# Kernel tuning notes

Hardware: AMD Instinct MI355X
Metric: run time of the kernel (lower is better)

## Reference

```python
import jax, jax.numpy as jnp
import numpy as np

N_NODES = 100000
N_EDGES = 1600000
D_IN = 128
D_HID = 128
N_CLS = 40


def setup_inputs() -> dict:
    key = jax.random.key(0)
    ks = jax.random.split(key, 8)
    x = jax.random.normal(ks[0], (N_NODES, D_IN), dtype=jnp.float32)
    edge_index = jax.random.randint(ks[1], (2, N_EDGES), 0, N_NODES, dtype=jnp.int64)
    s = 1.0 / np.sqrt(D_IN)
    W1_l = jax.random.normal(ks[2], (D_IN, D_HID), dtype=jnp.float32) * s
    W1_r = jax.random.normal(ks[3], (D_IN, D_HID), dtype=jnp.float32) * s
    b1 = jnp.zeros((D_HID,), dtype=jnp.float32)
    s2 = 1.0 / np.sqrt(D_HID)
    W2_l = jax.random.normal(ks[4], (D_HID, N_CLS), dtype=jnp.float32) * s2
    W2_r = jax.random.normal(ks[5], (D_HID, N_CLS), dtype=jnp.float32) * s2
    b2 = jnp.zeros((N_CLS,), dtype=jnp.float32)
    return {"x": x, "edge_index": edge_index, "W1_l": W1_l, "W1_r": W1_r,
            "b1": b1, "W2_l": W2_l, "W2_r": W2_r, "b2": b2}


def _sage_conv(x, src, dst, Wl, Wr, b):
    # mean-aggregate neighbor features (PyG SAGEConv, aggr='mean')
    n = x.shape[0]
    agg = jax.ops.segment_sum(x[src], dst, num_segments=n)           # [N, d]
    deg = jax.ops.segment_sum(jnp.ones_like(dst, dtype=x.dtype), dst, num_segments=n)
    mean = agg / jnp.maximum(deg, 1.0)[:, None]
    # lin_l(mean) + bias + lin_r(x_root)  (lin_r has no bias in PyG)
    return mean @ Wl + b + x @ Wr


def reference(x, edge_index, W1_l, W1_r, b1, W2_l, W2_r, b2):
    src, dst = edge_index[0], edge_index[1]
    h = jax.nn.relu(_sage_conv(x, src, dst, W1_l, W1_r, b1))
    # F.dropout(training=...) is identity in eval mode (deterministic reference)
    out = _sage_conv(h, src, dst, W2_l, W2_r, b2)
    return jax.nn.softmax(out, axis=1)
```

## Files before the change

### kernel.cpp

```cpp
#include <hip/hip_runtime.h>

#define DIM 128
#define NCLS 40
#define NBIN 256
#define BINSH 9
#define CHUNK 4096

typedef unsigned short ushort_t;
typedef __attribute__((ext_vector_type(8))) short bf16x8;
typedef __attribute__((ext_vector_type(4))) float f32x4;
typedef __attribute__((ext_vector_type(4))) unsigned uint4a;

__device__ __forceinline__ ushort_t f2b(float f) {
    union { float f; unsigned u; } v; v.f = f;
    unsigned r = v.u + 0x7FFFu + ((v.u >> 16) & 1u);
    return (ushort_t)(r >> 16);
}

__device__ __forceinline__ float b2f(ushort_t b) {
    union { unsigned u; float f; } v; v.u = ((unsigned)b) << 16;
    return v.f;
}

__device__ __forceinline__ void acc_fp8x4(float4& a, int w) {
    a.x += __builtin_amdgcn_cvt_f32_fp8(w, 0);
    a.y += __builtin_amdgcn_cvt_f32_fp8(w, 1);
    a.z += __builtin_amdgcn_cvt_f32_fp8(w, 2);
    a.w += __builtin_amdgcn_cvt_f32_fp8(w, 3);
}

__device__ __forceinline__ void acc_pair(float& a, float& b, unsigned u) {
    union { unsigned x; float f; } lo, hi;
    lo.x = u << 16;
    hi.x = u & 0xFFFF0000u;
    a += lo.f;
    b += hi.f;
}

__global__ __launch_bounds__(256) void prep_kernel(
    const float* __restrict__ x, ushort_t* __restrict__ xbf, unsigned* __restrict__ xq,
    const float* __restrict__ W1r, const float* __restrict__ W1l, ushort_t* __restrict__ Wp,
    const float* __restrict__ W2l, ushort_t* __restrict__ Wp2,
    int* __restrict__ binCnt, int n4, int cb)
{
    const int b = blockIdx.x;
    if (b < cb) {
        int i = b * 256 + threadIdx.x;
        if (i >= n4) return;
        f32x4 v = __builtin_nontemporal_load(((const f32x4*)x) + i);
        ushort4 o;
        o.x = f2b(v.x); o.y = f2b(v.y); o.z = f2b(v.z); o.w = f2b(v.w);
        ((ushort4*)xbf)[i] = o;
        int p = __builtin_amdgcn_cvt_pk_fp8_f32(v.x, v.y, 0, false);
        p = __builtin_amdgcn_cvt_pk_fp8_f32(v.z, v.w, p, true);
        xq[i] = (unsigned)p;
    } else if (b < cb + 128) {
        int o = (b - cb) * 256 + threadIdx.x;
        int j    = o & 7;
        int lane = (o >> 3) & 63;
        int t    = (o >> 9) & 7;
        int kc   = o >> 12;
        int k = kc * 32 + (lane >> 4) * 8 + j;
        int nn = t * 16 + (lane & 15);
        float v = (k < DIM) ? W1r[k * DIM + nn] : W1l[(k - DIM) * DIM + nn];
        Wp[o] = f2b(v);
    } else if (b < cb + 152) {
        int o = (b - cb - 128) * 256 + threadIdx.x;
        int j    = o & 7;
        int lane = (o >> 3) & 63;
        int rem  = o >> 9;
        int t    = rem % 3;
        int kc   = rem / 3;
        int k  = kc * 32 + (lane >> 4) * 8 + j;
        int nn = t * 16 + (lane & 15);
        Wp2[o] = (nn < NCLS) ? f2b(W2l[k * NCLS + nn]) : (ushort_t)0;
    } else {
        binCnt[threadIdx.x] = 0;
    }
}


__global__ __launch_bounds__(256) void bincount_kernel(const int* __restrict__ dst,
                                                       int* __restrict__ binCnt, int E) {
    __shared__ int hist[NBIN];
    hist[threadIdx.x] = 0;
    __syncthreads();
    const int tid = blockIdx.x * 256 + threadIdx.x;
    const int stride = gridDim.x * 256;
    for (int e = tid; e < E; e += stride)
        atomicAdd(&hist[__builtin_nontemporal_load(dst + e) >> BINSH], 1);
    __syncthreads();
    if (hist[threadIdx.x]) atomicAdd(&binCnt[threadIdx.x], hist[threadIdx.x]);
}

__global__ __launch_bounds__(NBIN) void binscan_kernel(const int* __restrict__ binCnt,
                                                       int* __restrict__ binBase,
                                                       int* __restrict__ binCtr,
                                                       int* __restrict__ row_ptr, int n) {
    __shared__ int sc[NBIN];
    const int t = threadIdx.x;
    sc[t] = binCnt[t];
    __syncthreads();
    for (int off = 1; off < NBIN; off <<= 1) {
        int v = (t >= off) ? sc[t - off] : 0;
        __syncthreads();
        sc[t] += v;
        __syncthreads();
    }
    int excl = (t == 0) ? 0 : sc[t - 1];
    binBase[t] = excl;
    binCtr[t]  = excl;
    if (t == NBIN - 1) { binBase[NBIN] = sc[t]; row_ptr[n] = sc[t]; }
}

__global__ __launch_bounds__(256) void binscatter_kernel(
    const int* __restrict__ src, const int* __restrict__ dst,
    int* __restrict__ binCtr, int2* __restrict__ pairs, int E)
{
    __shared__ int ss[CHUNK];
    __shared__ int sd[CHUNK];
    __shared__ int hist[NBIN];
    __shared__ int base[NBIN];
    __shared__ int cnt[NBIN];
    const int nchunk = (E + CHUNK - 1) / CHUNK;
    for (int c = blockIdx.x; c < nchunk; c += gridDim.x) {
        const int e0 = c * CHUNK;
        const int m = min(CHUNK, E - e0);
        for (int i = threadIdx.x; i < m; i += 256) {
            ss[i] = __builtin_nontemporal_load(src + e0 + i);
            sd[i] = __builtin_nontemporal_load(dst + e0 + i);
        }
        hist[threadIdx.x] = 0;
        cnt[threadIdx.x] = 0;
        __syncthreads();
        for (int i = threadIdx.x; i < m; i += 256)
            atomicAdd(&hist[sd[i] >> BINSH], 1);
        __syncthreads();
        base[threadIdx.x] = hist[threadIdx.x]
            ? atomicAdd(&binCtr[threadIdx.x], hist[threadIdx.x]) : 0;
        __syncthreads();
        for (int i = threadIdx.x; i < m; i += 256) {
            int d = sd[i];
            int b = d >> BINSH;
            int off = base[b] + atomicAdd(&cnt[b], 1);
            pairs[off] = make_int2(ss[i], d);
        }
        __syncthreads();
    }
}

__global__ __launch_bounds__(256) void bincsr_kernel(
    const int2* __restrict__ pairs, const int* __restrict__ binBase,
    int* __restrict__ row_ptr, int* __restrict__ eidx, int n)
{
    __shared__ int deg[512];
    __shared__ int sc[512];
    __shared__ int cnt[512];
    const int b  = blockIdx.x;
    const int lo = binBase[b];
    const int hi = binBase[b + 1];
    const int nlo = b << BINSH;
    const int t = threadIdx.x;
    deg[t] = 0; deg[t + 256] = 0;
    cnt[t] = 0; cnt[t + 256] = 0;
    __syncthreads();
    for (int e = lo + t; e < hi; e += 256) {
        int2 p = pairs[e];
        atomicAdd(&deg[p.y - nlo], 1);
    }
    __syncthreads();
    sc[t] = deg[t];
    sc[t + 256] = deg[t + 256];
    __syncthreads();
    for (int off = 1; off < 512; off <<= 1) {
        int v0 = (t >= off) ? sc[t - off] : 0;
        int v1 = sc[t + 256 - off];
        __syncthreads();
        sc[t] += v0;
        sc[t + 256] += v1;
        __syncthreads();
    }
    {
        int node0 = nlo + t;
        int node1 = nlo + t + 256;
        if (node0 < n) row_ptr[node0] = lo + sc[t] - deg[t];
        if (node1 < n) row_ptr[node1] = lo + sc[t + 256] - deg[t + 256];
    }
    for (int e = lo + t; e < hi; e += 256) {
        int2 p = pairs[e];
        int dl = p.y - nlo;
        int slot = sc[dl] - deg[dl] + atomicAdd(&cnt[dl], 1);
        eidx[lo + slot] = p.x;
    }
}


__global__ __launch_bounds__(256) void gather128_kernel(
    const unsigned* __restrict__ xq, const int* __restrict__ row_ptr,
    const int* __restrict__ eidx, ushort_t* __restrict__ Bbf, int n)
{
    int t = blockIdx.x * 256 + threadIdx.x;
    int node = t >> 5;
    if (node >= n) return;
    int q = t & 31;
    int j  = row_ptr[node];
    int je = row_ptr[node + 1];
    const float id = 1.0f / fmaxf((float)(je - j), 1.0f);
    float4 acc = make_float4(0.f, 0.f, 0.f, 0.f);
    for (; j + 3 < je; j += 4) {
        int s0 = eidx[j], s1 = eidx[j + 1], s2 = eidx[j + 2], s3 = eidx[j + 3];
        int w0 = (int)xq[(size_t)s0 * 32 + q];
        int w1 = (int)xq[(size_t)s1 * 32 + q];
        int w2 = (int)xq[(size_t)s2 * 32 + q];
        int w3 = (int)xq[(size_t)s3 * 32 + q];
        acc_fp8x4(acc, w0); acc_fp8x4(acc, w1);
        acc_fp8x4(acc, w2); acc_fp8x4(acc, w3);
    }
    for (; j < je; ++j) {
        int s0 = eidx[j];
        acc_fp8x4(acc, (int)xq[(size_t)s0 * 32 + q]);
    }
    ushort4 o;
    o.x = f2b(acc.x * id); o.y = f2b(acc.y * id);
    o.z = f2b(acc.z * id); o.w = f2b(acc.w * id);
    ((ushort4*)(Bbf + (size_t)node * DIM))[q] = o;
}

__global__ __launch_bounds__(256) void mfma_gemm_kernel(
    const ushort_t* __restrict__ xbf, const ushort_t* __restrict__ mxbf,
    const ushort_t* __restrict__ Wp, const ushort_t* __restrict__ Wp2,
    const float* __restrict__ bias,
    ushort_t* __restrict__ Hbf, ushort_t* __restrict__ Cbf, int n)
{
    __shared__ ushort_t hl[4][16 * 136];
    const int wave = threadIdx.x >> 6;
    const int lane = threadIdx.x & 63;
    const int m16  = lane & 15;
    const int quad = lane >> 4;
    const int row0 = blockIdx.x * 64 + wave * 16;
    int arow = row0 + m16;
    if (arow >= n) arow = n - 1;
    f32x4 acc[8];
    #pragma unroll
    for (int t = 0; t < 8; ++t) acc[t] = (f32x4){0.f, 0.f, 0.f, 0.f};
    const ushort_t* __restrict__ xrow = xbf  + (size_t)arow * DIM;
    const ushort_t* __restrict__ mrow = mxbf + (size_t)arow * DIM;
    #pragma unroll
    for (int kc = 0; kc < 8; ++kc) {
        const int kcol = (kc & 3) * 32 + quad * 8;
        const bf16x8 afrag = *(const bf16x8*)((kc < 4 ? xrow : mrow) + kcol);
        const ushort_t* __restrict__ wp = Wp + (size_t)kc * 4096 + (size_t)lane * 8;
        #pragma unroll
        for (int t = 0; t < 8; ++t) {
            const bf16x8 bfrag = *(const bf16x8*)(wp + (size_t)t * 512);
            acc[t] = __builtin_amdgcn_mfma_f32_16x16x32_bf16(afrag, bfrag, acc[t], 0, 0, 0);
        }
    }
    ushort_t* __restrict__ hw = hl[wave];
    #pragma unroll
    for (int t = 0; t < 8; ++t) {
        const int col = t * 16 + m16;
        const float bv = bias[col];
        #pragma unroll
        for (int r = 0; r < 4; ++r) {
            hw[(quad * 4 + r) * 136 + col] = f2b(fmaxf(acc[t][r] + bv, 0.f));
        }
    }
    f32x4 acc2[3];
    #pragma unroll
    for (int t = 0; t < 3; ++t) acc2[t] = (f32x4){0.f, 0.f, 0.f, 0.f};
    const bool rowok = (row0 + m16) < n;
    #pragma unroll
    for (int kc = 0; kc < 4; ++kc) {
        const bf16x8 afrag2 = *(const bf16x8*)(hw + m16 * 136 + kc * 32 + quad * 8);
        if (rowok)
            *(bf16x8*)(Hbf + (size_t)(row0 + m16) * DIM + kc * 32 + quad * 8) = afrag2;
        const ushort_t* __restrict__ wp2 = Wp2 + (size_t)kc * 1536 + (size_t)lane * 8;
        #pragma unroll
        for (int t = 0; t < 3; ++t) {
            const bf16x8 bfrag = *(const bf16x8*)(wp2 + (size_t)t * 512);
            acc2[t] = __builtin_amdgcn_mfma_f32_16x16x32_bf16(afrag2, bfrag, acc2[t], 0, 0, 0);
        }
    }
    #pragma unroll
    for (int t = 0; t < 3; ++t) {
        const int col = t * 16 + m16;
        if (col >= NCLS) continue;
        #pragma unroll
        for (int r = 0; r < 4; ++r) {
            const int row = row0 + quad * 4 + r;
            if (row < n) Cbf[(size_t)row * NCLS + col] = f2b(acc2[t][r]);
        }
    }
}

__global__ __launch_bounds__(256) void final_kernel(
    const ushort_t* __restrict__ Hbf, const ushort_t* __restrict__ Cbf,
    const int* __restrict__ row_ptr, const int* __restrict__ eidx,
    const float* __restrict__ W, const float* __restrict__ b2,
    float* __restrict__ out, int n)
{
    __shared__ float lgs[64][41];
    const int tid  = threadIdx.x;
    const int q    = tid >> 6;
    const int lane = tid & 63;
    const int r    = lane & 3;
    const int na   = q * 16 + (lane >> 2);
    const int nodeA = blockIdx.x * 64 + na;
    float lg[40];
    #pragma unroll
    for (int c = 0; c < 40; ++c) lg[c] = 0.f;
    if (nodeA < n) {
        int j  = row_ptr[nodeA] + r;
        int je = row_ptr[nodeA + 1];
        for (; j < je; j += 4) {
            int s = eidx[j];
            const uint4a* __restrict__ p = (const uint4a*)(Cbf + (size_t)s * NCLS);
            uint4a v0 = p[0], v1 = p[1], v2 = p[2], v3 = p[3], v4 = p[4];
            acc_pair(lg[0],  lg[1],  v0.x); acc_pair(lg[2],  lg[3],  v0.y);
            acc_pair(lg[4],  lg[5],  v0.z); acc_pair(lg[6],  lg[7],  v0.w);
            acc_pair(lg[8],  lg[9],  v1.x); acc_pair(lg[10], lg[11], v1.y);
            acc_pair(lg[12], lg[13], v1.z); acc_pair(lg[14], lg[15], v1.w);
            acc_pair(lg[16], lg[17], v2.x); acc_pair(lg[18], lg[19], v2.y);
            acc_pair(lg[20], lg[21], v2.z); acc_pair(lg[22], lg[23], v2.w);
            acc_pair(lg[24], lg[25], v3.x); acc_pair(lg[26], lg[27], v3.y);
            acc_pair(lg[28], lg[29], v3.z); acc_pair(lg[30], lg[31], v3.w);
            acc_pair(lg[32], lg[33], v4.x); acc_pair(lg[34], lg[35], v4.y);
            acc_pair(lg[36], lg[37], v4.z); acc_pair(lg[38], lg[39], v4.w);
        }
    }
    const bool hi1 = (lane & 1) != 0;
    float h20[20];
    #pragma unroll
    for (int i = 0; i < 20; ++i) {
        float sendv = hi1 ? lg[i] : lg[20 + i];
        float recv  = __shfl_xor(sendv, 1, 64);
        h20[i] = (hi1 ? lg[20 + i] : lg[i]) + recv;
    }
    const bool hi2 = (lane & 2) != 0;
    float h10[10];
    #pragma unroll
    for (int i = 0; i < 10; ++i) {
        float sendv = hi2 ? h20[i] : h20[10 + i];
        float recv  = __shfl_xor(sendv, 2, 64);
        h10[i] = (hi2 ? h20[10 + i] : h20[i]) + recv;
    }
    const int cbase = (hi1 ? 20 : 0) + (hi2 ? 10 : 0);
    #pragma unroll
    for (int i = 0; i < 10; ++i) lgs[na][cbase + i] = h10[i];
    __syncthreads();
    const int c0 = __builtin_amdgcn_readfirstlane(q * 10);
    const int node = blockIdx.x * 64 + lane;
    if (node < n) {
        const float dg = (float)(row_ptr[node + 1] - row_ptr[node]);
        const float id = 1.0f / fmaxf(dg, 1.0f);
        float lgd[10];
        #pragma unroll
        for (int c = 0; c < 10; ++c) lgd[c] = fmaf(lgs[lane][c0 + c], id, b2[c0 + c]);
        const ushort_t* __restrict__ h = Hbf + (size_t)node * DIM;
        for (int k = 0; k < DIM; k += 4) {
            const ushort4 hu = *(const ushort4*)(h + k);
            const float hx = b2f(hu.x), hy = b2f(hu.y), hz = b2f(hu.z), hw = b2f(hu.w);
            const float* __restrict__ w0 = W + (size_t)(k + 0) * NCLS + c0;
            const float* __restrict__ w1 = W + (size_t)(k + 1) * NCLS + c0;
            const float* __restrict__ w2 = W + (size_t)(k + 2) * NCLS + c0;
            const float* __restrict__ w3 = W + (size_t)(k + 3) * NCLS + c0;
            #pragma unroll
            for (int c = 0; c < 10; ++c) {
                float a = lgd[c];
                a = fmaf(hx, w0[c], a);
                a = fmaf(hy, w1[c], a);
                a = fmaf(hz, w2[c], a);
                a = fmaf(hw, w3[c], a);
                lgd[c] = a;
            }
        }
        #pragma unroll
        for (int c = 0; c < 10; ++c) lgs[lane][c0 + c] = lgd[c];
    }
    __syncthreads();
    if (q == 0 && node < n) {
        float v[NCLS];
        #pragma unroll
        for (int c = 0; c < NCLS; ++c) v[c] = lgs[lane][c];
        float m = v[0];
        #pragma unroll
        for (int c = 1; c < NCLS; ++c) m = fmaxf(m, v[c]);
        float s = 0.f;
        #pragma unroll
        for (int c = 0; c < NCLS; ++c) { v[c] = __expf(v[c] - m); s += v[c]; }
        const float inv = 1.0f / s;
        float* __restrict__ o = out + (size_t)node * NCLS;
        #pragma unroll
        for (int c = 0; c < NCLS; ++c) o[c] = v[c] * inv;
    }
}

extern "C" void kernel_launch(void* const* d_in, const int* in_sizes, int n_in,
                              void* d_out, int out_size, void* d_ws, size_t ws_size,
                              hipStream_t stream) {
    const float* x   = (const float*)d_in[0];
    const int*   ei  = (const int*)d_in[1];
    const float* W1l = (const float*)d_in[2];
    const float* W1r = (const float*)d_in[3];
    const float* b1  = (const float*)d_in[4];
    const float* W2l = (const float*)d_in[5];
    const float* W2r = (const float*)d_in[6];
    const float* b2  = (const float*)d_in[7];
    float* out = (float*)d_out;

    const int n = in_sizes[0] / DIM;
    const int E = in_sizes[1] / 2;
    const int* src = ei;
    const int* dst = ei + E;

    ushort_t* xbf     = (ushort_t*)d_ws;
    ushort_t* mxbf    = xbf + (size_t)n * DIM;
    ushort_t* Hbf     = mxbf + (size_t)n * DIM;
    ushort_t* Cbf     = Hbf + (size_t)n * DIM;
    unsigned* xq      = (unsigned*)(Cbf + (size_t)n * NCLS);
    ushort_t* Wp      = (ushort_t*)(xq + (size_t)n * 32);
    ushort_t* Wp2     = Wp + 256 * DIM;
    int*      eidx    = (int*)(Wp2 + 4 * 1536);
    int2*     pairs   = (int2*)(eidx + E);
    int*      row_ptr = (int*)(pairs + E);
    int*      binCnt  = row_ptr + (n + 1);
    int*      binBase = binCnt + NBIN;
    int*      binCtr  = binBase + NBIN + 1;

    const int n4 = n * 32;
    const int cb = (n4 + 255) / 256;
    prep_kernel<<<cb + 153, 256, 0, stream>>>(x, xbf, xq, W1r, W1l, Wp,
                                              W2l, Wp2, binCnt, n4, cb);

    bincount_kernel  <<<512, 256, 0, stream>>>(dst, binCnt, E);
    binscan_kernel   <<<1, NBIN, 0, stream>>>(binCnt, binBase, binCtr, row_ptr, n);
    binscatter_kernel<<<512, 256, 0, stream>>>(src, dst, binCtr, pairs, E);
    bincsr_kernel    <<<NBIN, 256, 0, stream>>>(pairs, binBase, row_ptr, eidx, n);

    {
        long long t = (long long)n * 32;
        gather128_kernel<<<(int)((t + 255) / 256), 256, 0, stream>>>(xq, row_ptr, eidx, mxbf, n);
    }
    mfma_gemm_kernel<<<(n + 63) / 64, 256, 0, stream>>>(xbf, mxbf, Wp, Wp2, b1, Hbf, Cbf, n);

    final_kernel<<<(n + 63) / 64, 256, 0, stream>>>(Hbf, Cbf, row_ptr, eidx, W2r, b2, out, n);
}
```

Before: 308.6 us.

## Fuse layer-1 neighbor gather into MFMA GEMM and widen final kernel to 512 threads

Removes the standalone gather kernel and computes the fp8 mean aggregation directly inside the GEMM kernel, staging the bf16 mean rows in shared memory instead of writing and rereading them through global memory. Each node is now handled by 4 lanes using 32-byte vector loads per neighbor, which coalesces less than the old 32-lanes-per-node layout and lowers parallelism in the gather phase. Separately, the final kernel moves to 512 threads with 8 lanes per node for the edge reduction, adding a third shuffle stage and giving each wave 5 output classes in the dense part.

```diff
diff --git a/kernel.cpp b/kernel.cpp
--- a/kernel.cpp
+++ b/kernel.cpp
@@ -22,11 +22,11 @@
     return v.f;
 }
 
-__device__ __forceinline__ void acc_fp8x4(float4& a, int w) {
-    a.x += __builtin_amdgcn_cvt_f32_fp8(w, 0);
-    a.y += __builtin_amdgcn_cvt_f32_fp8(w, 1);
-    a.z += __builtin_amdgcn_cvt_f32_fp8(w, 2);
-    a.w += __builtin_amdgcn_cvt_f32_fp8(w, 3);
+__device__ __forceinline__ void acc_fp8x4(float4& a, unsigned w) {
+    a.x += __builtin_amdgcn_cvt_f32_fp8((int)w, 0);
+    a.y += __builtin_amdgcn_cvt_f32_fp8((int)w, 1);
+    a.z += __builtin_amdgcn_cvt_f32_fp8((int)w, 2);
+    a.w += __builtin_amdgcn_cvt_f32_fp8((int)w, 3);
 }
 
 __device__ __forceinline__ void acc_pair(float& a, float& b, unsigned u) {
@@ -195,39 +195,9 @@
 }
 
 
-__global__ __launch_bounds__(256) void gather128_kernel(
-    const unsigned* __restrict__ xq, const int* __restrict__ row_ptr,
-    const int* __restrict__ eidx, ushort_t* __restrict__ Bbf, int n)
-{
-    int t = blockIdx.x * 256 + threadIdx.x;
-    int node = t >> 5;
-    if (node >= n) return;
-    int q = t & 31;
-    int j  = row_ptr[node];
-    int je = row_ptr[node + 1];
-    const float id = 1.0f / fmaxf((float)(je - j), 1.0f);
-    float4 acc = make_float4(0.f, 0.f, 0.f, 0.f);
-    for (; j + 3 < je; j += 4) {
-        int s0 = eidx[j], s1 = eidx[j + 1], s2 = eidx[j + 2], s3 = eidx[j + 3];
-        int w0 = (int)xq[(size_t)s0 * 32 + q];
-        int w1 = (int)xq[(size_t)s1 * 32 + q];
-        int w2 = (int)xq[(size_t)s2 * 32 + q];
-        int w3 = (int)xq[(size_t)s3 * 32 + q];
-        acc_fp8x4(acc, w0); acc_fp8x4(acc, w1);
-        acc_fp8x4(acc, w2); acc_fp8x4(acc, w3);
-    }
-    for (; j < je; ++j) {
-        int s0 = eidx[j];
-        acc_fp8x4(acc, (int)xq[(size_t)s0 * 32 + q]);
-    }
-    ushort4 o;
-    o.x = f2b(acc.x * id); o.y = f2b(acc.y * id);
-    o.z = f2b(acc.z * id); o.w = f2b(acc.w * id);
-    ((ushort4*)(Bbf + (size_t)node * DIM))[q] = o;
-}
-
 __global__ __launch_bounds__(256) void mfma_gemm_kernel(
-    const ushort_t* __restrict__ xbf, const ushort_t* __restrict__ mxbf,
+    const ushort_t* __restrict__ xbf, const unsigned* __restrict__ xq,
+    const int* __restrict__ row_ptr, const int* __restrict__ eidx,
     const ushort_t* __restrict__ Wp, const ushort_t* __restrict__ Wp2,
     const float* __restrict__ bias,
     ushort_t* __restrict__ Hbf, ushort_t* __restrict__ Cbf, int n)
@@ -238,17 +208,67 @@
     const int m16  = lane & 15;
     const int quad = lane >> 4;
     const int row0 = blockIdx.x * 64 + wave * 16;
+    ushort_t* __restrict__ hw = hl[wave];
+
+    {
+        const int nl   = lane >> 2;
+        const int part = lane & 3;
+        const int node = row0 + nl;
+        float4 a[8];
+        #pragma unroll
+        for (int i = 0; i < 8; ++i) a[i] = make_float4(0.f, 0.f, 0.f, 0.f);
+        float id = 0.f;
+        if (node < n) {
+            int j  = row_ptr[node];
+            int je = row_ptr[node + 1];
+            id = 1.0f / fmaxf((float)(je - j), 1.0f);
+            for (; j + 1 < je; j += 2) {
+                int s0 = eidx[j], s1 = eidx[j + 1];
+                const uint4a* __restrict__ p0 = (const uint4a*)(xq + (size_t)s0 * 32 + part * 8);
+                const uint4a* __restrict__ p1 = (const uint4a*)(xq + (size_t)s1 * 32 + part * 8);
+                uint4a v0 = p0[0], v1 = p0[1];
+                uint4a w0 = p1[0], w1 = p1[1];
+                acc_fp8x4(a[0], v0.x); acc_fp8x4(a[1], v0.y);
+                acc_fp8x4(a[2], v0.z); acc_fp8x4(a[3], v0.w);
+                acc_fp8x4(a[4], v1.x); acc_fp8x4(a[5], v1.y);
+                acc_fp8x4(a[6], v1.z); acc_fp8x4(a[7], v1.w);
+                acc_fp8x4(a[0], w0.x); acc_fp8x4(a[1], w0.y);
+                acc_fp8x4(a[2], w0.z); acc_fp8x4(a[3], w0.w);
+                acc_fp8x4(a[4], w1.x); acc_fp8x4(a[5], w1.y);
+                acc_fp8x4(a[6], w1.z); acc_fp8x4(a[7], w1.w);
+            }
+            if (j < je) {
+                int s0 = eidx[j];
+                const uint4a* __restrict__ p0 = (const uint4a*)(xq + (size_t)s0 * 32 + part * 8);
+                uint4a v0 = p0[0], v1 = p0[1];
+                acc_fp8x4(a[0], v0.x); acc_fp8x4(a[1], v0.y);
+                acc_fp8x4(a[2], v0.z); acc_fp8x4(a[3], v0.w);
+                acc_fp8x4(a[4], v1.x); acc_fp8x4(a[5], v1.y);
+                acc_fp8x4(a[6], v1.z); acc_fp8x4(a[7], v1.w);
+            }
+        }
+        ushort_t* __restrict__ mrowl = hw + nl * 136 + part * 32;
+        #pragma unroll
+        for (int i = 0; i < 8; ++i) {
+            ushort4 o;
+            o.x = f2b(a[i].x * id); o.y = f2b(a[i].y * id);
+            o.z = f2b(a[i].z * id); o.w = f2b(a[i].w * id);
+            ((ushort4*)mrowl)[i] = o;
+        }
+    }
+
     int arow = row0 + m16;
     if (arow >= n) arow = n - 1;
     f32x4 acc[8];
     #pragma unroll
     for (int t = 0; t < 8; ++t) acc[t] = (f32x4){0.f, 0.f, 0.f, 0.f};
-    const ushort_t* __restrict__ xrow = xbf  + (size_t)arow * DIM;
-    const ushort_t* __restrict__ mrow = mxbf + (size_t)arow * DIM;
+    const ushort_t* __restrict__ xrow = xbf + (size_t)arow * DIM;
     #pragma unroll
     for (int kc = 0; kc < 8; ++kc) {
         const int kcol = (kc & 3) * 32 + quad * 8;
-        const bf16x8 afrag = *(const bf16x8*)((kc < 4 ? xrow : mrow) + kcol);
+        const bf16x8 afrag = (kc < 4)
+            ? *(const bf16x8*)(xrow + kcol)
+            : *(const bf16x8*)(hw + m16 * 136 + kcol);
         const ushort_t* __restrict__ wp = Wp + (size_t)kc * 4096 + (size_t)lane * 8;
         #pragma unroll
         for (int t = 0; t < 8; ++t) {
@@ -256,7 +276,6 @@
             acc[t] = __builtin_amdgcn_mfma_f32_16x16x32_bf16(afrag, bfrag, acc[t], 0, 0, 0);
         }
     }
-    ushort_t* __restrict__ hw = hl[wave];
     #pragma unroll
     for (int t = 0; t < 8; ++t) {
         const int col = t * 16 + m16;
@@ -294,7 +313,7 @@
     }
 }
 
-__global__ __launch_bounds__(256) void final_kernel(
+__global__ __launch_bounds__(512) void final_kernel(
     const ushort_t* __restrict__ Hbf, const ushort_t* __restrict__ Cbf,
     const int* __restrict__ row_ptr, const int* __restrict__ eidx,
     const float* __restrict__ W, const float* __restrict__ b2,
@@ -304,8 +323,8 @@
     const int tid  = threadIdx.x;
     const int q    = tid >> 6;
     const int lane = tid & 63;
-    const int r    = lane & 3;
-    const int na   = q * 16 + (lane >> 2);
+    const int r    = lane & 7;
+    const int na   = q * 8 + (lane >> 3);
     const int nodeA = blockIdx.x * 64 + na;
     float lg[40];
     #pragma unroll
@@ -313,7 +332,7 @@
     if (nodeA < n) {
         int j  = row_ptr[nodeA] + r;
         int je = row_ptr[nodeA + 1];
-        for (; j < je; j += 4) {
+        for (; j < je; j += 8) {
             int s = eidx[j];
             const uint4a* __restrict__ p = (const uint4a*)(Cbf + (size_t)s * NCLS);
             uint4a v0 = p[0], v1 = p[1], v2 = p[2], v3 = p[3], v4 = p[4];
@@ -345,18 +364,26 @@
         float recv  = __shfl_xor(sendv, 2, 64);
         h10[i] = (hi2 ? h20[10 + i] : h20[i]) + recv;
     }
-    const int cbase = (hi1 ? 20 : 0) + (hi2 ? 10 : 0);
-    #pragma unroll
-    for (int i = 0; i < 10; ++i) lgs[na][cbase + i] = h10[i];
-    __syncthreads();
-    const int c0 = __builtin_amdgcn_readfirstlane(q * 10);
+    const bool hi3 = (lane & 4) != 0;
+    float h5[5];
+    #pragma unroll
+    for (int i = 0; i < 5; ++i) {
+        float sendv = hi3 ? h10[i] : h10[5 + i];
+        float recv  = __shfl_xor(sendv, 4, 64);
+        h5[i] = (hi3 ? h10[5 + i] : h10[i]) + recv;
+    }
+    const int cbase = (hi1 ? 20 : 0) + (hi2 ? 10 : 0) + (hi3 ? 5 : 0);
+    #pragma unroll
+    for (int i = 0; i < 5; ++i) lgs[na][cbase + i] = h5[i];
+    __syncthreads();
+    const int c0 = __builtin_amdgcn_readfirstlane(q * 5);
     const int node = blockIdx.x * 64 + lane;
     if (node < n) {
         const float dg = (float)(row_ptr[node + 1] - row_ptr[node]);
         const float id = 1.0f / fmaxf(dg, 1.0f);
-        float lgd[10];
-        #pragma unroll
-        for (int c = 0; c < 10; ++c) lgd[c] = fmaf(lgs[lane][c0 + c], id, b2[c0 + c]);
+        float lgd[5];
+        #pragma unroll
+        for (int c = 0; c < 5; ++c) lgd[c] = fmaf(lgs[lane][c0 + c], id, b2[c0 + c]);
         const ushort_t* __restrict__ h = Hbf + (size_t)node * DIM;
         for (int k = 0; k < DIM; k += 4) {
             const ushort4 hu = *(const ushort4*)(h + k);
@@ -366,7 +393,7 @@
             const float* __restrict__ w2 = W + (size_t)(k + 2) * NCLS + c0;
             const float* __restrict__ w3 = W + (size_t)(k + 3) * NCLS + c0;
             #pragma unroll
-            for (int c = 0; c < 10; ++c) {
+            for (int c = 0; c < 5; ++c) {
                 float a = lgd[c];
                 a = fmaf(hx, w0[c], a);
                 a = fmaf(hy, w1[c], a);
@@ -376,7 +403,7 @@
             }
         }
         #pragma unroll
-        for (int c = 0; c < 10; ++c) lgs[lane][c0 + c] = lgd[c];
+        for (int c = 0; c < 5; ++c) lgs[lane][c0 + c] = lgd[c];
     }
     __syncthreads();
     if (q == 0 && node < n) {
@@ -427,6 +454,7 @@
     int*      binCnt  = row_ptr + (n + 1);
     int*      binBase = binCnt + NBIN;
     int*      binCtr  = binBase + NBIN + 1;
+    (void)mxbf;
 
     const int n4 = n * 32;
     const int cb = (n4 + 255) / 256;
@@ -438,11 +466,8 @@
     binscatter_kernel<<<512, 256, 0, stream>>>(src, dst, binCtr, pairs, E);
     bincsr_kernel    <<<NBIN, 256, 0, stream>>>(pairs, binBase, row_ptr, eidx, n);
 
-    {
-        long long t = (long long)n * 32;
-        gather128_kernel<<<(int)((t + 255) / 256), 256, 0, stream>>>(xq, row_ptr, eidx, mxbf, n);
-    }
-    mfma_gemm_kernel<<<(n + 63) / 64, 256, 0, stream>>>(xbf, mxbf, Wp, Wp2, b1, Hbf, Cbf, n);
-
-    final_kernel<<<(n + 63) / 64, 256, 0, stream>>>(Hbf, Cbf, row_ptr, eidx, W2r, b2, out, n);
-}
+    mfma_gemm_kernel<<<(n + 63) / 64, 256, 0, stream>>>(xbf, xq, row_ptr, eidx,
+                                                        Wp, Wp2, b1, Hbf, Cbf, n);
+
+    final_kernel<<<(n + 63) / 64, 512, 0, stream>>>(Hbf, Cbf, row_ptr, eidx, W2r, b2, out, n);
+}
```

New measurement: 335.0 us. +8.6%, slower.

## Build CSR via global per-node degree atomics instead of two-pass bin sort

Applied to the files above, without the earlier changes.

Replaces the bin-sort CSR construction (bin scatter into pairs, then per-bin local sort) with a per-node degree count using global atomics, a per-bin scan that produces row pointers and counters, and a direct atomic scatter of sources into eidx. This removes the intermediate pairs buffer and one full pass over the edges, cutting one kernel launch. In exchange it issues 1.6M global atomics twice on random addresses, and the neighbor order within each row becomes nondeterministic, which can change floating-point summation order.

```diff
diff --git a/kernel.cpp b/kernel.cpp
--- a/kernel.cpp
+++ b/kernel.cpp
@@ -4,7 +4,6 @@
 #define NCLS 40
 #define NBIN 256
 #define BINSH 9
-#define CHUNK 4096
 
 typedef unsigned short ushort_t;
 typedef __attribute__((ext_vector_type(8))) short bf16x8;
@@ -41,7 +40,7 @@
     const float* __restrict__ x, ushort_t* __restrict__ xbf, unsigned* __restrict__ xq,
     const float* __restrict__ W1r, const float* __restrict__ W1l, ushort_t* __restrict__ Wp,
     const float* __restrict__ W2l, ushort_t* __restrict__ Wp2,
-    int* __restrict__ binCnt, int n4, int cb)
+    int* __restrict__ binCnt, int* __restrict__ deg, int n4, int cb, int n)
 {
     const int b = blockIdx.x;
     if (b < cb) {
@@ -74,103 +73,56 @@
         int k  = kc * 32 + (lane >> 4) * 8 + j;
         int nn = t * 16 + (lane & 15);
         Wp2[o] = (nn < NCLS) ? f2b(W2l[k * NCLS + nn]) : (ushort_t)0;
+    } else if (b == cb + 152) {
+        binCnt[threadIdx.x] = 0;
     } else {
-        binCnt[threadIdx.x] = 0;
-    }
-}
-
-
-__global__ __launch_bounds__(256) void bincount_kernel(const int* __restrict__ dst,
+        int o = (b - cb - 153) * 256 + threadIdx.x;
+        if (o < n) deg[o] = 0;
+    }
+}
+
+
+__global__ __launch_bounds__(256) void degcount_kernel(const int* __restrict__ dst,
+                                                       int* __restrict__ deg,
                                                        int* __restrict__ binCnt, int E) {
     __shared__ int hist[NBIN];
     hist[threadIdx.x] = 0;
     __syncthreads();
     const int tid = blockIdx.x * 256 + threadIdx.x;
     const int stride = gridDim.x * 256;
-    for (int e = tid; e < E; e += stride)
-        atomicAdd(&hist[__builtin_nontemporal_load(dst + e) >> BINSH], 1);
+    for (int e = tid; e < E; e += stride) {
+        int d = __builtin_nontemporal_load(dst + e);
+        atomicAdd(&hist[d >> BINSH], 1);
+        atomicAdd(&deg[d], 1);
+    }
     __syncthreads();
     if (hist[threadIdx.x]) atomicAdd(&binCnt[threadIdx.x], hist[threadIdx.x]);
 }
 
-__global__ __launch_bounds__(NBIN) void binscan_kernel(const int* __restrict__ binCnt,
-                                                       int* __restrict__ binBase,
-                                                       int* __restrict__ binCtr,
-                                                       int* __restrict__ row_ptr, int n) {
-    __shared__ int sc[NBIN];
+__global__ __launch_bounds__(256) void rowptr_kernel(const int* __restrict__ binCnt,
+                                                     const int* __restrict__ deg,
+                                                     int* __restrict__ row_ptr,
+                                                     int* __restrict__ ctr, int n) {
+    __shared__ int bs[NBIN];
+    __shared__ int sc[512];
+    const int b = blockIdx.x;
     const int t = threadIdx.x;
-    sc[t] = binCnt[t];
+    bs[t] = binCnt[t];
     __syncthreads();
     for (int off = 1; off < NBIN; off <<= 1) {
-        int v = (t >= off) ? sc[t - off] : 0;
+        int v = (t >= off) ? bs[t - off] : 0;
         __syncthreads();
-        sc[t] += v;
+        bs[t] += v;
         __syncthreads();
     }
-    int excl = (t == 0) ? 0 : sc[t - 1];
-    binBase[t] = excl;
-    binCtr[t]  = excl;
-    if (t == NBIN - 1) { binBase[NBIN] = sc[t]; row_ptr[n] = sc[t]; }
-}
-
-__global__ __launch_bounds__(256) void binscatter_kernel(
-    const int* __restrict__ src, const int* __restrict__ dst,
-    int* __restrict__ binCtr, int2* __restrict__ pairs, int E)
-{
-    __shared__ int ss[CHUNK];
-    __shared__ int sd[CHUNK];
-    __shared__ int hist[NBIN];
-    __shared__ int base[NBIN];
-    __shared__ int cnt[NBIN];
-    const int nchunk = (E + CHUNK - 1) / CHUNK;
-    for (int c = blockIdx.x; c < nchunk; c += gridDim.x) {
-        const int e0 = c * CHUNK;
-        const int m = min(CHUNK, E - e0);
-        for (int i = threadIdx.x; i < m; i += 256) {
-            ss[i] = __builtin_nontemporal_load(src + e0 + i);
-            sd[i] = __builtin_nontemporal_load(dst + e0 + i);
-        }
-        hist[threadIdx.x] = 0;
-        cnt[threadIdx.x] = 0;
-        __syncthreads();
-        for (int i = threadIdx.x; i < m; i += 256)
-            atomicAdd(&hist[sd[i] >> BINSH], 1);
-        __syncthreads();
-        base[threadIdx.x] = hist[threadIdx.x]
-            ? atomicAdd(&binCtr[threadIdx.x], hist[threadIdx.x]) : 0;
-        __syncthreads();
-        for (int i = threadIdx.x; i < m; i += 256) {
-            int d = sd[i];
-            int b = d >> BINSH;
-            int off = base[b] + atomicAdd(&cnt[b], 1);
-            pairs[off] = make_int2(ss[i], d);
-        }
-        __syncthreads();
-    }
-}
-
-__global__ __launch_bounds__(256) void bincsr_kernel(
-    const int2* __restrict__ pairs, const int* __restrict__ binBase,
-    int* __restrict__ row_ptr, int* __restrict__ eidx, int n)
-{
-    __shared__ int deg[512];
-    __shared__ int sc[512];
-    __shared__ int cnt[512];
-    const int b  = blockIdx.x;
-    const int lo = binBase[b];
-    const int hi = binBase[b + 1];
+    const int base = (b == 0) ? 0 : bs[b - 1];
     const int nlo = b << BINSH;
-    const int t = threadIdx.x;
-    deg[t] = 0; deg[t + 256] = 0;
-    cnt[t] = 0; cnt[t + 256] = 0;
-    __syncthreads();
-    for (int e = lo + t; e < hi; e += 256) {
-        int2 p = pairs[e];
-        atomicAdd(&deg[p.y - nlo], 1);
-    }
-    __syncthreads();
-    sc[t] = deg[t];
-    sc[t + 256] = deg[t + 256];
+    const int n0 = nlo + t;
+    const int n1 = nlo + 256 + t;
+    const int d0 = (n0 < n) ? deg[n0] : 0;
+    const int d1 = (n1 < n) ? deg[n1] : 0;
+    sc[t] = d0;
+    sc[t + 256] = d1;
     __syncthreads();
     for (int off = 1; off < 512; off <<= 1) {
         int v0 = (t >= off) ? sc[t - off] : 0;
@@ -180,17 +132,22 @@
         sc[t + 256] += v1;
         __syncthreads();
     }
-    {
-        int node0 = nlo + t;
-        int node1 = nlo + t + 256;
-        if (node0 < n) row_ptr[node0] = lo + sc[t] - deg[t];
-        if (node1 < n) row_ptr[node1] = lo + sc[t + 256] - deg[t + 256];
-    }
-    for (int e = lo + t; e < hi; e += 256) {
-        int2 p = pairs[e];
-        int dl = p.y - nlo;
-        int slot = sc[dl] - deg[dl] + atomicAdd(&cnt[dl], 1);
-        eidx[lo + slot] = p.x;
+    if (n0 < n) { int v = base + sc[t] - d0;       row_ptr[n0] = v; ctr[n0] = v; }
+    if (n1 < n) { int v = base + sc[t + 256] - d1; row_ptr[n1] = v; ctr[n1] = v; }
+    if (b == (int)gridDim.x - 1 && t == 255) row_ptr[n] = base + sc[511];
+}
+
+__global__ __launch_bounds__(256) void scatter_kernel(const int* __restrict__ src,
+                                                      const int* __restrict__ dst,
+                                                      int* __restrict__ ctr,
+                                                      int* __restrict__ eidx, int E) {
+    const int tid = blockIdx.x * 256 + threadIdx.x;
+    const int stride = gridDim.x * 256;
+    for (int e = tid; e < E; e += stride) {
+        int d = __builtin_nontemporal_load(dst + e);
+        int s = __builtin_nontemporal_load(src + e);
+        int slot = atomicAdd(&ctr[d], 1);
+        eidx[slot] = s;
     }
 }
 
@@ -422,21 +379,20 @@
     ushort_t* Wp      = (ushort_t*)(xq + (size_t)n * 32);
     ushort_t* Wp2     = Wp + 256 * DIM;
     int*      eidx    = (int*)(Wp2 + 4 * 1536);
-    int2*     pairs   = (int2*)(eidx + E);
-    int*      row_ptr = (int*)(pairs + E);
+    int*      deg     = eidx + E;
+    int*      ctr     = deg + n;
+    int*      row_ptr = ctr + n;
     int*      binCnt  = row_ptr + (n + 1);
-    int*      binBase = binCnt + NBIN;
-    int*      binCtr  = binBase + NBIN + 1;
 
     const int n4 = n * 32;
     const int cb = (n4 + 255) / 256;
-    prep_kernel<<<cb + 153, 256, 0, stream>>>(x, xbf, xq, W1r, W1l, Wp,
-                                              W2l, Wp2, binCnt, n4, cb);
-
-    bincount_kernel  <<<512, 256, 0, stream>>>(dst, binCnt, E);
-    binscan_kernel   <<<1, NBIN, 0, stream>>>(binCnt, binBase, binCtr, row_ptr, n);
-    binscatter_kernel<<<512, 256, 0, stream>>>(src, dst, binCtr, pairs, E);
-    bincsr_kernel    <<<NBIN, 256, 0, stream>>>(pairs, binBase, row_ptr, eidx, n);
+    const int zb = (n + 255) / 256;
+    prep_kernel<<<cb + 153 + zb, 256, 0, stream>>>(x, xbf, xq, W1r, W1l, Wp,
+                                                   W2l, Wp2, binCnt, deg, n4, cb, n);
+
+    degcount_kernel<<<512, 256, 0, stream>>>(dst, deg, binCnt, E);
+    rowptr_kernel  <<<NBIN, 256, 0, stream>>>(binCnt, deg, row_ptr, ctr, n);
+    scatter_kernel <<<2048, 256, 0, stream>>>(src, dst, ctr, eidx, E);
 
     {
         long long t = (long long)n * 32;
```

Measured after the change: 419.7 us. 1.36x slower.

## Fold bin scan into scatter/CSR kernels, pack edge pairs, pad class rows

Applied to the files above, without the earlier changes.

Removes the single-block binscan launch by recomputing the 256-bin prefix sum redundantly inside every binscatter and bincsr block. Intermediate pairs are packed into a 32-bit word (9-bit local dst, 17-bit src), which halves pair traffic. The layer-2 logits buffer is padded to a 64-element row stride so gathered rows start on 128-byte boundaries. The trade-off is redundant scan work in every block and an assumption that node ids fit in 17 bits.

```diff
diff --git a/kernel.cpp b/kernel.cpp
--- a/kernel.cpp
+++ b/kernel.cpp
@@ -2,6 +2,7 @@
 
 #define DIM 128
 #define NCLS 40
+#define CPAD 64
 #define NBIN 256
 #define BINSH 9
 #define CHUNK 4096
@@ -41,7 +42,7 @@
     const float* __restrict__ x, ushort_t* __restrict__ xbf, unsigned* __restrict__ xq,
     const float* __restrict__ W1r, const float* __restrict__ W1l, ushort_t* __restrict__ Wp,
     const float* __restrict__ W2l, ushort_t* __restrict__ Wp2,
-    int* __restrict__ binCnt, int n4, int cb)
+    int* __restrict__ binCnt, int* __restrict__ binCtr, int n4, int cb)
 {
     const int b = blockIdx.x;
     if (b < cb) {
@@ -76,6 +77,7 @@
         Wp2[o] = (nn < NCLS) ? f2b(W2l[k * NCLS + nn]) : (ushort_t)0;
     } else {
         binCnt[threadIdx.x] = 0;
+        binCtr[threadIdx.x] = 0;
     }
 }
 
@@ -93,81 +95,82 @@
     if (hist[threadIdx.x]) atomicAdd(&binCnt[threadIdx.x], hist[threadIdx.x]);
 }
 
-__global__ __launch_bounds__(NBIN) void binscan_kernel(const int* __restrict__ binCnt,
-                                                       int* __restrict__ binBase,
-                                                       int* __restrict__ binCtr,
-                                                       int* __restrict__ row_ptr, int n) {
-    __shared__ int sc[NBIN];
-    const int t = threadIdx.x;
-    sc[t] = binCnt[t];
-    __syncthreads();
-    for (int off = 1; off < NBIN; off <<= 1) {
-        int v = (t >= off) ? sc[t - off] : 0;
-        __syncthreads();
-        sc[t] += v;
-        __syncthreads();
-    }
-    int excl = (t == 0) ? 0 : sc[t - 1];
-    binBase[t] = excl;
-    binCtr[t]  = excl;
-    if (t == NBIN - 1) { binBase[NBIN] = sc[t]; row_ptr[n] = sc[t]; }
-}
-
 __global__ __launch_bounds__(256) void binscatter_kernel(
     const int* __restrict__ src, const int* __restrict__ dst,
-    int* __restrict__ binCtr, int2* __restrict__ pairs, int E)
+    const int* __restrict__ binCnt, int* __restrict__ binCtr,
+    unsigned* __restrict__ pairs, int E)
 {
     __shared__ int ss[CHUNK];
     __shared__ int sd[CHUNK];
+    __shared__ int excl[NBIN];
     __shared__ int hist[NBIN];
     __shared__ int base[NBIN];
     __shared__ int cnt[NBIN];
+    const int t = threadIdx.x;
+    excl[t] = binCnt[t];
+    __syncthreads();
+    for (int off = 1; off < NBIN; off <<= 1) {
+        int v = (t >= off) ? excl[t - off] : 0;
+        __syncthreads();
+        excl[t] += v;
+        __syncthreads();
+    }
+    const int mybase = (t == 0) ? 0 : excl[t - 1];
+    __syncthreads();
+    excl[t] = mybase;
+    __syncthreads();
     const int nchunk = (E + CHUNK - 1) / CHUNK;
     for (int c = blockIdx.x; c < nchunk; c += gridDim.x) {
         const int e0 = c * CHUNK;
         const int m = min(CHUNK, E - e0);
-        for (int i = threadIdx.x; i < m; i += 256) {
+        for (int i = t; i < m; i += 256) {
             ss[i] = __builtin_nontemporal_load(src + e0 + i);
             sd[i] = __builtin_nontemporal_load(dst + e0 + i);
         }
-        hist[threadIdx.x] = 0;
-        cnt[threadIdx.x] = 0;
-        __syncthreads();
-        for (int i = threadIdx.x; i < m; i += 256)
+        hist[t] = 0;
+        cnt[t] = 0;
+        __syncthreads();
+        for (int i = t; i < m; i += 256)
             atomicAdd(&hist[sd[i] >> BINSH], 1);
         __syncthreads();
-        base[threadIdx.x] = hist[threadIdx.x]
-            ? atomicAdd(&binCtr[threadIdx.x], hist[threadIdx.x]) : 0;
-        __syncthreads();
-        for (int i = threadIdx.x; i < m; i += 256) {
+        base[t] = hist[t] ? (excl[t] + atomicAdd(&binCtr[t], hist[t])) : 0;
+        __syncthreads();
+        for (int i = t; i < m; i += 256) {
             int d = sd[i];
             int b = d >> BINSH;
             int off = base[b] + atomicAdd(&cnt[b], 1);
-            pairs[off] = make_int2(ss[i], d);
+            pairs[off] = ((unsigned)(d & ((1 << BINSH) - 1)) << 17) | (unsigned)ss[i];
         }
         __syncthreads();
     }
 }
 
 __global__ __launch_bounds__(256) void bincsr_kernel(
-    const int2* __restrict__ pairs, const int* __restrict__ binBase,
-    int* __restrict__ row_ptr, int* __restrict__ eidx, int n)
-{
+    const unsigned* __restrict__ pairs, const int* __restrict__ binCnt,
+    int* __restrict__ row_ptr, int* __restrict__ eidx, int n, int E)
+{
+    __shared__ int bs[NBIN];
     __shared__ int deg[512];
     __shared__ int sc[512];
     __shared__ int cnt[512];
     const int b  = blockIdx.x;
-    const int lo = binBase[b];
-    const int hi = binBase[b + 1];
+    const int t = threadIdx.x;
+    bs[t] = binCnt[t];
+    __syncthreads();
+    for (int off = 1; off < NBIN; off <<= 1) {
+        int v = (t >= off) ? bs[t - off] : 0;
+        __syncthreads();
+        bs[t] += v;
+        __syncthreads();
+    }
+    const int lo = (b == 0) ? 0 : bs[b - 1];
+    const int hi = bs[b];
     const int nlo = b << BINSH;
-    const int t = threadIdx.x;
     deg[t] = 0; deg[t + 256] = 0;
     cnt[t] = 0; cnt[t + 256] = 0;
     __syncthreads();
-    for (int e = lo + t; e < hi; e += 256) {
-        int2 p = pairs[e];
-        atomicAdd(&deg[p.y - nlo], 1);
-    }
+    for (int e = lo + t; e < hi; e += 256)
+        atomicAdd(&deg[pairs[e] >> 17], 1);
     __syncthreads();
     sc[t] = deg[t];
     sc[t + 256] = deg[t + 256];
@@ -186,11 +189,12 @@
         if (node0 < n) row_ptr[node0] = lo + sc[t] - deg[t];
         if (node1 < n) row_ptr[node1] = lo + sc[t + 256] - deg[t + 256];
     }
+    if (b == NBIN - 1 && t == 255) row_ptr[n] = E;
     for (int e = lo + t; e < hi; e += 256) {
-        int2 p = pairs[e];
-        int dl = p.y - nlo;
+        unsigned p = pairs[e];
+        int dl = p >> 17;
         int slot = sc[dl] - deg[dl] + atomicAdd(&cnt[dl], 1);
-        eidx[lo + slot] = p.x;
+        eidx[lo + slot] = (int)(p & 0x1FFFFu);
     }
 }
 
@@ -289,7 +293,7 @@
         #pragma unroll
         for (int r = 0; r < 4; ++r) {
             const int row = row0 + quad * 4 + r;
-            if (row < n) Cbf[(size_t)row * NCLS + col] = f2b(acc2[t][r]);
+            if (row < n) Cbf[(size_t)row * CPAD + col] = f2b(acc2[t][r]);
         }
     }
 }
@@ -315,7 +319,7 @@
         int je = row_ptr[nodeA + 1];
         for (; j < je; j += 4) {
             int s = eidx[j];
-            const uint4a* __restrict__ p = (const uint4a*)(Cbf + (size_t)s * NCLS);
+            const uint4a* __restrict__ p = (const uint4a*)(Cbf + (size_t)s * CPAD);
             uint4a v0 = p[0], v1 = p[1], v2 = p[2], v3 = p[3], v4 = p[4];
             acc_pair(lg[0],  lg[1],  v0.x); acc_pair(lg[2],  lg[3],  v0.y);
             acc_pair(lg[4],  lg[5],  v0.z); acc_pair(lg[6],  lg[7],  v0.w);
@@ -418,25 +422,23 @@
     ushort_t* mxbf    = xbf + (size_t)n * DIM;
     ushort_t* Hbf     = mxbf + (size_t)n * DIM;
     ushort_t* Cbf     = Hbf + (size_t)n * DIM;
-    unsigned* xq      = (unsigned*)(Cbf + (size_t)n * NCLS);
+    unsigned* xq      = (unsigned*)(Cbf + (size_t)n * CPAD);
     ushort_t* Wp      = (ushort_t*)(xq + (size_t)n * 32);
     ushort_t* Wp2     = Wp + 256 * DIM;
     int*      eidx    = (int*)(Wp2 + 4 * 1536);
-    int2*     pairs   = (int2*)(eidx + E);
+    unsigned* pairs   = (unsigned*)(eidx + E);
     int*      row_ptr = (int*)(pairs + E);
     int*      binCnt  = row_ptr + (n + 1);
-    int*      binBase = binCnt + NBIN;
-    int*      binCtr  = binBase + NBIN + 1;
+    int*      binCtr  = binCnt + NBIN;
 
     const int n4 = n * 32;
     const int cb = (n4 + 255) / 256;
     prep_kernel<<<cb + 153, 256, 0, stream>>>(x, xbf, xq, W1r, W1l, Wp,
-                                              W2l, Wp2, binCnt, n4, cb);
+                                              W2l, Wp2, binCnt, binCtr, n4, cb);
 
     bincount_kernel  <<<512, 256, 0, stream>>>(dst, binCnt, E);
-    binscan_kernel   <<<1, NBIN, 0, stream>>>(binCnt, binBase, binCtr, row_ptr, n);
-    binscatter_kernel<<<512, 256, 0, stream>>>(src, dst, binCtr, pairs, E);
-    bincsr_kernel    <<<NBIN, 256, 0, stream>>>(pairs, binBase, row_ptr, eidx, n);
+    binscatter_kernel<<<512, 256, 0, stream>>>(src, dst, binCnt, binCtr, pairs, E);
+    bincsr_kernel    <<<NBIN, 256, 0, stream>>>(pairs, binCnt, row_ptr, eidx, n, E);
 
     {
         long long t = (long long)n * 32;
```

Result: no change. 302.6 us (-1.9%).
